# Kernel optimization log

Hardware: AMD Instinct MI355X
Metric: run time of the kernel (lower is better)

## Reference

```python
import jax, jax.numpy as jnp
import numpy as np

DECAY = 0.99
EPSILON = 1e-05
CODEBOOK_SIZE = 1024
DIM = 128


def setup_inputs() -> dict:
    key = jax.random.key(0)
    k1, k2, k3, k4 = jax.random.split(key, 4)
    x = jax.random.normal(k1, (8, 8192, DIM), dtype=jnp.float32)
    embed = jax.random.normal(k2, (CODEBOOK_SIZE, DIM), dtype=jnp.float32)
    cluster_size = jax.random.uniform(k3, (CODEBOOK_SIZE,), dtype=jnp.float32)
    embed_avg = jax.random.normal(k4, (CODEBOOK_SIZE, DIM), dtype=jnp.float32)
    return {"x": x, "embed": embed, "cluster_size": cluster_size, "embed_avg": embed_avg}


def reference(x, embed, cluster_size, embed_avg):
    shape = x.shape
    flat = x.reshape(-1, shape[-1])  # [N, dim]

    # quantize: negative squared euclidean distance, argmax == nearest code
    dist = -(jnp.sum(flat * flat, axis=1, keepdims=True)
             - 2.0 * flat @ embed.T
             + jnp.sum(embed * embed, axis=1)[None, :])  # [N, K]
    embed_ind = jnp.argmax(dist, axis=-1)  # [N]

    quantize = embed[embed_ind].reshape(shape)            # dequantize
    embed_ind_out = embed_ind.reshape(shape[:-1])

    # training-time EMA updates (one-hot expressed as segment_sum)
    batch_cluster_size = jax.ops.segment_sum(
        jnp.ones_like(embed_ind, dtype=flat.dtype), embed_ind,
        num_segments=CODEBOOK_SIZE)                       # == one_hot.sum(0)
    new_cluster_size = cluster_size * DECAY + (1.0 - DECAY) * batch_cluster_size

    embed_sum = jax.ops.segment_sum(flat, embed_ind,
                                    num_segments=CODEBOOK_SIZE)  # == (x.T @ one_hot).T
    new_embed_avg = embed_avg * DECAY + (1.0 - DECAY) * embed_sum

    total = new_cluster_size.sum()
    smoothed = (new_cluster_size + EPSILON) / (total + CODEBOOK_SIZE * EPSILON)
    smoothed_counts = smoothed * total
    new_embed = new_embed_avg / smoothed_counts[:, None]

    return quantize, embed_ind_out, new_cluster_size, new_embed_avg, new_embed
```

## Files before the change

### kernel.cpp

```cpp
#include <hip/hip_runtime.h>
#include <math.h>

#define DIM 128
#define KCODES 1024
#define NROWS 65536

typedef short bf16x8 __attribute__((ext_vector_type(8)));
typedef float f32x4 __attribute__((ext_vector_type(4)));

#define WS_COUNTS 0
#define WS_ESUM   1024
#define WS_IOFF   132096
#define WS_TOTAL  133120
#define WS_ENORM2 133124
#define WS_EBF    134148
#define WS_WIN    461828
#define WS_SORTED 527364
#define WS_SCODE  592900

#define OFF_Q   0
#define OFF_IND 8388608
#define OFF_NCS 8454144
#define OFF_NEA 8455168
#define OFF_NE  8586240

#define LDST 136

static __device__ __forceinline__ unsigned short f2bf(float f) {
    unsigned u = __float_as_uint(f);
    unsigned r = (u + 0x7FFFu + ((u >> 16) & 1u)) >> 16;
    return (unsigned short)r;
}

__global__ __launch_bounds__(64) void k_prep(const float* __restrict__ embed,
                                             unsigned short* __restrict__ ebf,
                                             float* __restrict__ en2,
                                             float* __restrict__ counts,
                                             float* __restrict__ esum) {
    int k = blockIdx.x;
    int l = threadIdx.x;
    if (l == 0) counts[k] = 0.0f;
    *(float2*)&esum[(size_t)k * DIM + l * 2] = (float2){0.0f, 0.0f};
    float2 v = *(const float2*)&embed[(size_t)k * DIM + l * 2];
    ushort2 b;
    b.x = f2bf(v.x);
    b.y = f2bf(v.y);
    *(ushort2*)&ebf[k * DIM + l * 2] = b;
    float s = v.x * v.x + v.y * v.y;
    #pragma unroll
    for (int off = 32; off; off >>= 1) s += __shfl_xor(s, off);
    if (l == 0) en2[k] = 512.0f - 0.5f * s;
}

__global__ __launch_bounds__(512, 4) void k_fused(const float* __restrict__ x,
                                                  const float* __restrict__ embed,
                                                  const unsigned short* __restrict__ ebf,
                                                  const float* __restrict__ en2g,
                                                  int* __restrict__ win_g,
                                                  float* __restrict__ counts,
                                                  float* __restrict__ out) {
    __shared__ unsigned short buf[2][128 * LDST];
    __shared__ float en2s[KCODES];
    __shared__ int winS[128];

    const int tid = threadIdx.x;
    const int row0 = blockIdx.x * 128;

    #pragma unroll
    for (int i = 0; i < 2; ++i) en2s[i * 512 + tid] = en2g[i * 512 + tid];

    #pragma unroll
    for (int i = 0; i < 8; ++i) {
        int idx4 = i * 512 + tid;
        int lin = idx4 * 4;
        int r = lin >> 7, d = lin & 127;
        float4 v = *(const float4*)&x[(size_t)(row0 + r) * DIM + d];
        ushort4 b;
        b.x = f2bf(v.x); b.y = f2bf(v.y); b.z = f2bf(v.z); b.w = f2bf(v.w);
        *(ushort4*)&buf[0][r * LDST + d] = b;
    }
    __syncthreads();

    const int lane = tid & 63;
    const int wv = tid >> 6;
    const int ch = wv & 1;
    const int rh = (wv >> 1) * 32;
    const int l15 = lane & 15;
    const int q = lane >> 4;

    bf16x8 af[4][2];
    #pragma unroll
    for (int ks = 0; ks < 4; ++ks)
        #pragma unroll
        for (int t = 0; t < 2; ++t)
            af[ks][t] = *(const bf16x8*)&buf[0][(rh + t * 16 + l15) * LDST + ks * 32 + q * 8];

    uint4 er[4];
    #pragma unroll
    for (int i = 0; i < 4; ++i) {
        int idx8 = i * 512 + tid;
        int r = idx8 >> 4;
        int d = (idx8 & 15) * 8;
        er[i] = *(const uint4*)&ebf[(size_t)r * DIM + d];
    }
    #pragma unroll
    for (int i = 0; i < 4; ++i) {
        int idx8 = i * 512 + tid;
        int r = idx8 >> 4;
        int d = (idx8 & 15) * 8;
        *(uint4*)&buf[1][r * LDST + d] = er[i];
    }
    __syncthreads();

    float m1[2][4], m2[2][4];
    #pragma unroll
    for (int a = 0; a < 2; ++a)
        #pragma unroll
        for (int b = 0; b < 4; ++b) { m1[a][b] = 0.0f; m2[a][b] = 0.0f; }

    for (int ct = 0; ct < 8; ++ct) {
        const int c0 = ct * 128;
        const unsigned short* cbuf = buf[1 ^ (ct & 1)];

        if (ct < 7) {
            #pragma unroll
            for (int i = 0; i < 4; ++i) {
                int idx8 = i * 512 + tid;
                int r = idx8 >> 4;
                int d = (idx8 & 15) * 8;
                er[i] = *(const uint4*)&ebf[(size_t)(c0 + 128 + r) * DIM + d];
            }
        }

        f32x4 acc[2][4];
        #pragma unroll
        for (int cl = 0; cl < 4; ++cl) {
            float en = en2s[c0 + ch * 64 + cl * 16 + l15];
            #pragma unroll
            for (int rt = 0; rt < 2; ++rt) acc[rt][cl] = (f32x4){en, en, en, en};
        }

        #pragma unroll
        for (int ks = 0; ks < 4; ++ks) {
            bf16x8 bfr[4];
            #pragma unroll
            for (int cl = 0; cl < 4; ++cl)
                bfr[cl] = *(const bf16x8*)&cbuf[(ch * 64 + cl * 16 + l15) * LDST + ks * 32 + q * 8];
            #pragma unroll
            for (int rt = 0; rt < 2; ++rt)
                #pragma unroll
                for (int cl = 0; cl < 4; ++cl)
                    acc[rt][cl] = __builtin_amdgcn_mfma_f32_16x16x32_bf16(af[ks][rt], bfr[cl],
                                                                          acc[rt][cl], 0, 0, 0);
        }

        #pragma unroll
        for (int cl = 0; cl < 4; ++cl) {
            unsigned cu = (unsigned)(c0 + ch * 64 + cl * 16 + l15);
            #pragma unroll
            for (int rt = 0; rt < 2; ++rt)
                #pragma unroll
                for (int rg = 0; rg < 4; ++rg) {
                    float s = acc[rt][cl][rg];
                    float kf = __uint_as_float((__float_as_uint(s) & ~1023u) | cu);
                    m2[rt][rg] = __builtin_amdgcn_fmed3f(m1[rt][rg], m2[rt][rg], kf);
                    m1[rt][rg] = fmaxf(m1[rt][rg], kf);
                }
        }

        if (ct < 7) {
            unsigned short* nbuf = buf[ct & 1];
            #pragma unroll
            for (int i = 0; i < 4; ++i) {
                int idx8 = i * 512 + tid;
                int r = idx8 >> 4;
                int d = (idx8 & 15) * 8;
                *(uint4*)&nbuf[r * LDST + d] = er[i];
            }
        }
        __syncthreads();
    }

    float* scratch = (float*)buf[0];
    unsigned* hist = (unsigned*)buf[0] + 512;

    #pragma unroll
    for (int rt = 0; rt < 2; ++rt)
        #pragma unroll
        for (int rg = 0; rg < 4; ++rg) {
            float a1 = m1[rt][rg], a2 = m2[rt][rg];
            #pragma unroll
            for (int off = 1; off <= 8; off <<= 1) {
                float o1 = __shfl_xor(a1, off);
                float o2 = __shfl_xor(a2, off);
                float t = fmaxf(a2, o2);
                a2 = __builtin_amdgcn_fmed3f(a1, o1, t);
                a1 = fmaxf(a1, o1);
            }
            if (l15 == 0) {
                int row = rh + rt * 16 + q * 4 + rg;
                scratch[row * 4 + ch * 2 + 0] = a1;
                scratch[row * 4 + ch * 2 + 1] = a2;
            }
        }

    #pragma unroll
    for (int i = 0; i < 2; ++i) hist[i * 512 + tid] = 0u;
    __syncthreads();

    {
        const int sub = tid & 15;
        const int g = tid >> 4;
        #pragma unroll 2
        for (int rr = 0; rr < 4; ++rr) {
            const int lrow = g * 4 + rr;
            const float* sp = &scratch[lrow * 4];
            int ci[4];
            ci[0] = (int)(__float_as_uint(sp[0]) & 1023u);
            ci[1] = (int)(__float_as_uint(sp[1]) & 1023u);
            ci[2] = (int)(__float_as_uint(sp[2]) & 1023u);
            ci[3] = (int)(__float_as_uint(sp[3]) & 1023u);

            const float* xr = &x[(size_t)(row0 + lrow) * DIM + sub * 4];
            float4 xa = *(const float4*)xr;
            float4 xb = *(const float4*)(xr + 64);

            double d[4];
            #pragma unroll
            for (int j = 0; j < 4; ++j) {
                const float* er2 = &embed[(size_t)ci[j] * DIM + sub * 4];
                float4 ea4 = *(const float4*)er2;
                float4 eb4 = *(const float4*)(er2 + 64);
                double t0 = (double)xa.x - (double)ea4.x;
                double t1 = (double)xa.y - (double)ea4.y;
                double t2 = (double)xa.z - (double)ea4.z;
                double t3 = (double)xa.w - (double)ea4.w;
                double t4 = (double)xb.x - (double)eb4.x;
                double t5 = (double)xb.y - (double)eb4.y;
                double t6 = (double)xb.z - (double)eb4.z;
                double t7 = (double)xb.w - (double)eb4.w;
                d[j] = ((t0 * t0 + t1 * t1) + (t2 * t2 + t3 * t3)) +
                       ((t4 * t4 + t5 * t5) + (t6 * t6 + t7 * t7));
            }
            #pragma unroll
            for (int off = 1; off <= 8; off <<= 1) {
                #pragma unroll
                for (int j = 0; j < 4; ++j) d[j] += __shfl_xor(d[j], off);
            }

            int win = ci[0];
            double dw = d[0];
            #pragma unroll
            for (int j = 1; j < 4; ++j) {
                bool b = (d[j] < dw) || (d[j] == dw && ci[j] < win);
                dw = b ? d[j] : dw;
                win = b ? ci[j] : win;
            }
            if (sub == 0) winS[lrow] = win;
        }
    }
    __syncthreads();

    if (tid < 128) {
        int w = winS[tid];
        atomicAdd(&hist[w], 1u);
        win_g[row0 + tid] = w;
        out[OFF_IND + row0 + tid] = (float)w;
    }

    #pragma unroll 4
    for (int i = 0; i < 16; ++i) {
        int lrow = wv * 16 + i;
        int w = winS[lrow];
        float2 v = *(const float2*)&embed[(size_t)w * DIM + lane * 2];
        *(float2*)&out[OFF_Q + (size_t)(row0 + lrow) * DIM + lane * 2] = v;
    }

    __syncthreads();
    #pragma unroll
    for (int i = 0; i < 2; ++i) {
        unsigned c = hist[i * 512 + tid];
        if (c) atomicAdd(&counts[i * 512 + tid], (float)c);
    }
}

__global__ __launch_bounds__(1024) void k_offsets(const float* __restrict__ cs,
                                                  float* __restrict__ out,
                                                  float* __restrict__ ws) {
    __shared__ int wsum[16];
    __shared__ float wtot[16];
    const float* counts = ws + WS_COUNTS;
    int* ioff = (int*)(ws + WS_IOFF);

    int t = threadIdx.x;
    int lane = t & 63, w = t >> 6;
    float cf = counts[t];
    int c = (int)cf;
    float ncs = cs[t] * 0.99f + 0.01f * cf;
    out[OFF_NCS + t] = ncs;

    int v = c;
    #pragma unroll
    for (int off = 1; off < 64; off <<= 1) {
        int o = __shfl_up(v, off);
        if (lane >= off) v += o;
    }
    float nf = ncs;
    #pragma unroll
    for (int off = 32; off; off >>= 1) nf += __shfl_xor(nf, off);

    if (lane == 63) wsum[w] = v;
    if (lane == 0) wtot[w] = nf;
    __syncthreads();

    int base = 0;
    for (int i = 0; i < w; ++i) base += wsum[i];
    ioff[t] = base + v - c;

    if (t == 0) {
        float tt = 0.f;
        for (int i = 0; i < 16; ++i) tt += wtot[i];
        ws[WS_TOTAL] = tt;
    }
}

__global__ __launch_bounds__(1024) void k_sortscatter(const int* __restrict__ win_arr,
                                                      int* __restrict__ ioff,
                                                      int* __restrict__ sorted,
                                                      int* __restrict__ scode) {
    __shared__ int h[KCODES];
    __shared__ int bs[KCODES];
    const int t = threadIdx.x;
    h[t] = 0;
    __syncthreads();
    const int row = blockIdx.x * 1024 + t;
    const int w = win_arr[row];
    const int r = atomicAdd(&h[w], 1);
    __syncthreads();
    const int c = h[t];
    if (c) bs[t] = atomicAdd(&ioff[t], c);
    __syncthreads();
    const int pos = bs[w] + r;
    sorted[pos] = row;
    scode[pos] = w;
}

__global__ __launch_bounds__(256) void k_segsum(const float* __restrict__ x,
                                                const int* __restrict__ sorted,
                                                const int* __restrict__ scode,
                                                float* __restrict__ esum) {
    const int lane = threadIdx.x & 63;
    const int wv = threadIdx.x >> 6;
    const int base = blockIdx.x * 256 + wv * 64;
    const int l15 = lane & 15;

    float ax = 0.f, ay = 0.f;
    int cur = -1;

    #pragma unroll
    for (int cc = 0; cc < 4; ++cc) {
        const int p = base + cc * 16 + l15;
        const int srow = sorted[p];
        const int sc = scode[p];
        if (cc == 0) cur = __shfl(sc, 0);
        #pragma unroll
        for (int j = 0; j < 16; ++j) {
            int row = __shfl(srow, j);
            int c = __shfl(sc, j);
            if (c != cur) {
                atomicAdd(&esum[cur * DIM + lane * 2], ax);
                atomicAdd(&esum[cur * DIM + lane * 2 + 1], ay);
                ax = 0.f; ay = 0.f;
                cur = c;
            }
            float2 v = *(const float2*)&x[(size_t)row * DIM + lane * 2];
            ax += v.x;
            ay += v.y;
        }
    }
    atomicAdd(&esum[cur * DIM + lane * 2], ax);
    atomicAdd(&esum[cur * DIM + lane * 2 + 1], ay);
}

__global__ __launch_bounds__(256) void k_embed(const float* __restrict__ ea,
                                               const float* __restrict__ ws,
                                               float* __restrict__ out) {
    int i = blockIdx.x * 256 + threadIdx.x;
    int k = i >> 7;
    float nea = ea[i] * 0.99f + 0.01f * ws[WS_ESUM + i];
    out[OFF_NEA + i] = nea;
    float total = ws[WS_TOTAL];
    float ncs = out[OFF_NCS + k];
    float sm = (ncs + 1e-5f) / (total + 1024.0f * 1e-5f);
    out[OFF_NE + i] = nea / (sm * total);
}

extern "C" void kernel_launch(void* const* d_in, const int* in_sizes, int n_in,
                              void* d_out, int out_size, void* d_ws, size_t ws_size,
                              hipStream_t stream) {
    const float* x     = (const float*)d_in[0];
    const float* embed = (const float*)d_in[1];
    const float* cs    = (const float*)d_in[2];
    const float* ea    = (const float*)d_in[3];
    float* out = (float*)d_out;
    float* ws  = (float*)d_ws;

    k_prep<<<KCODES, 64, 0, stream>>>(embed, (unsigned short*)(ws + WS_EBF),
                                      ws + WS_ENORM2, ws + WS_COUNTS, ws + WS_ESUM);
    k_fused<<<NROWS / 128, 512, 0, stream>>>(x, embed,
                                             (const unsigned short*)(ws + WS_EBF),
                                             ws + WS_ENORM2, (int*)(ws + WS_WIN),
                                             ws + WS_COUNTS, out);
    k_offsets<<<1, 1024, 0, stream>>>(cs, out, ws);
    k_sortscatter<<<NROWS / 1024, 1024, 0, stream>>>((const int*)(ws + WS_WIN),
                                                     (int*)(ws + WS_IOFF),
                                                     (int*)(ws + WS_SORTED),
                                                     (int*)(ws + WS_SCODE));
    k_segsum<<<NROWS / 256, 256, 0, stream>>>(x, (const int*)(ws + WS_SORTED),
                                              (const int*)(ws + WS_SCODE), ws + WS_ESUM);
    k_embed<<<131072 / 256, 256, 0, stream>>>(ea, ws, out);
}
```

Measured before the change: 162.1 us.

## Swizzle LDS layout, pair argmax updates, and fuse offset scan into sort scatter

```diff
diff --git a/kernel.cpp b/kernel.cpp
--- a/kernel.cpp
+++ b/kernel.cpp
@@ -24,8 +24,6 @@
 #define OFF_NEA 8455168
 #define OFF_NE  8586240
 
-#define LDST 136
-
 static __device__ __forceinline__ unsigned short f2bf(float f) {
     unsigned u = __float_as_uint(f);
     unsigned r = (u + 0x7FFFu + ((u >> 16) & 1u)) >> 16;
@@ -36,10 +34,11 @@
                                              unsigned short* __restrict__ ebf,
                                              float* __restrict__ en2,
                                              float* __restrict__ counts,
-                                             float* __restrict__ esum) {
+                                             float* __restrict__ esum,
+                                             int* __restrict__ cursor) {
     int k = blockIdx.x;
     int l = threadIdx.x;
-    if (l == 0) counts[k] = 0.0f;
+    if (l == 0) { counts[k] = 0.0f; cursor[k] = 0; }
     *(float2*)&esum[(size_t)k * DIM + l * 2] = (float2){0.0f, 0.0f};
     float2 v = *(const float2*)&embed[(size_t)k * DIM + l * 2];
     ushort2 b;
@@ -59,7 +58,7 @@
                                                   int* __restrict__ win_g,
                                                   float* __restrict__ counts,
                                                   float* __restrict__ out) {
-    __shared__ unsigned short buf[2][128 * LDST];
+    __shared__ unsigned short buf[2][128 * 128];
     __shared__ float en2s[KCODES];
     __shared__ int winS[128];
 
@@ -77,7 +76,7 @@
         float4 v = *(const float4*)&x[(size_t)(row0 + r) * DIM + d];
         ushort4 b;
         b.x = f2bf(v.x); b.y = f2bf(v.y); b.z = f2bf(v.z); b.w = f2bf(v.w);
-        *(ushort4*)&buf[0][r * LDST + d] = b;
+        *(ushort4*)&buf[0][(r * 128 + d) ^ ((r & 7) << 3)] = b;
     }
     __syncthreads();
 
@@ -87,13 +86,14 @@
     const int rh = (wv >> 1) * 32;
     const int l15 = lane & 15;
     const int q = lane >> 4;
+    const int swz = (l15 & 7) << 3;
 
     bf16x8 af[4][2];
     #pragma unroll
     for (int ks = 0; ks < 4; ++ks)
         #pragma unroll
         for (int t = 0; t < 2; ++t)
-            af[ks][t] = *(const bf16x8*)&buf[0][(rh + t * 16 + l15) * LDST + ks * 32 + q * 8];
+            af[ks][t] = *(const bf16x8*)&buf[0][((rh + t * 16 + l15) * 128 + ks * 32 + q * 8) ^ swz];
 
     uint4 er[4];
     #pragma unroll
@@ -108,7 +108,7 @@
         int idx8 = i * 512 + tid;
         int r = idx8 >> 4;
         int d = (idx8 & 15) * 8;
-        *(uint4*)&buf[1][r * LDST + d] = er[i];
+        *(uint4*)&buf[1][(r * 128 + d) ^ ((r & 7) << 3)] = er[i];
     }
     __syncthreads();
 
@@ -140,12 +140,13 @@
             for (int rt = 0; rt < 2; ++rt) acc[rt][cl] = (f32x4){en, en, en, en};
         }
 
+        __builtin_amdgcn_s_setprio(1);
         #pragma unroll
         for (int ks = 0; ks < 4; ++ks) {
             bf16x8 bfr[4];
             #pragma unroll
             for (int cl = 0; cl < 4; ++cl)
-                bfr[cl] = *(const bf16x8*)&cbuf[(ch * 64 + cl * 16 + l15) * LDST + ks * 32 + q * 8];
+                bfr[cl] = *(const bf16x8*)&cbuf[((ch * 64 + cl * 16 + l15) * 128 + ks * 32 + q * 8) ^ swz];
             #pragma unroll
             for (int rt = 0; rt < 2; ++rt)
                 #pragma unroll
@@ -155,18 +156,23 @@
         }
 
         #pragma unroll
-        for (int cl = 0; cl < 4; ++cl) {
-            unsigned cu = (unsigned)(c0 + ch * 64 + cl * 16 + l15);
+        for (int cp = 0; cp < 2; ++cp) {
+            unsigned cu0 = (unsigned)(c0 + ch * 64 + cp * 32 + l15);
+            unsigned cu1 = cu0 + 16u;
             #pragma unroll
             for (int rt = 0; rt < 2; ++rt)
                 #pragma unroll
                 for (int rg = 0; rg < 4; ++rg) {
-                    float s = acc[rt][cl][rg];
-                    float kf = __uint_as_float((__float_as_uint(s) & ~1023u) | cu);
-                    m2[rt][rg] = __builtin_amdgcn_fmed3f(m1[rt][rg], m2[rt][rg], kf);
-                    m1[rt][rg] = fmaxf(m1[rt][rg], kf);
+                    float sa = acc[rt][cp * 2][rg];
+                    float sb = acc[rt][cp * 2 + 1][rg];
+                    float a = __uint_as_float((__float_as_uint(sa) & ~1023u) | cu0);
+                    float b = __uint_as_float((__float_as_uint(sb) & ~1023u) | cu1);
+                    m2[rt][rg] = fmaxf(m2[rt][rg],
+                                       __builtin_amdgcn_fmed3f(a, b, m1[rt][rg]));
+                    m1[rt][rg] = fmaxf(fmaxf(a, b), m1[rt][rg]);
                 }
         }
+        __builtin_amdgcn_s_setprio(0);
 
         if (ct < 7) {
             unsigned short* nbuf = buf[ct & 1];
@@ -175,7 +181,7 @@
                 int idx8 = i * 512 + tid;
                 int r = idx8 >> 4;
                 int d = (idx8 & 15) * 8;
-                *(uint4*)&nbuf[r * LDST + d] = er[i];
+                *(uint4*)&nbuf[(r * 128 + d) ^ ((r & 7) << 3)] = er[i];
             }
         }
         __syncthreads();
@@ -284,61 +290,58 @@
     }
 }
 
-__global__ __launch_bounds__(1024) void k_offsets(const float* __restrict__ cs,
-                                                  float* __restrict__ out,
-                                                  float* __restrict__ ws) {
+__global__ __launch_bounds__(1024) void k_scansort(const float* __restrict__ cs,
+                                                   const int* __restrict__ win_arr,
+                                                   float* __restrict__ ws,
+                                                   int* __restrict__ sorted,
+                                                   int* __restrict__ scode,
+                                                   float* __restrict__ out) {
+    __shared__ int h[KCODES];
+    __shared__ int bs[KCODES];
     __shared__ int wsum[16];
     __shared__ float wtot[16];
     const float* counts = ws + WS_COUNTS;
-    int* ioff = (int*)(ws + WS_IOFF);
-
-    int t = threadIdx.x;
-    int lane = t & 63, w = t >> 6;
-    float cf = counts[t];
-    int c = (int)cf;
-    float ncs = cs[t] * 0.99f + 0.01f * cf;
-    out[OFF_NCS + t] = ncs;
-
+    int* cursor = (int*)(ws + WS_IOFF);
+
+    const int t = threadIdx.x;
+    h[t] = 0;
+    __syncthreads();
+    const int row = blockIdx.x * 1024 + t;
+    const int w = win_arr[row];
+    const int r = atomicAdd(&h[w], 1);
+
+    const int lane = t & 63, wvi = t >> 6;
+    const float cf = counts[t];
+    const int c = (int)cf;
     int v = c;
     #pragma unroll
     for (int off = 1; off < 64; off <<= 1) {
         int o = __shfl_up(v, off);
         if (lane >= off) v += o;
     }
-    float nf = ncs;
-    #pragma unroll
-    for (int off = 32; off; off >>= 1) nf += __shfl_xor(nf, off);
-
-    if (lane == 63) wsum[w] = v;
-    if (lane == 0) wtot[w] = nf;
+    if (lane == 63) wsum[wvi] = v;
+    if (blockIdx.x == 0) {
+        float ncs = cs[t] * 0.99f + 0.01f * cf;
+        out[OFF_NCS + t] = ncs;
+        float nf = ncs;
+        #pragma unroll
+        for (int off = 32; off; off >>= 1) nf += __shfl_xor(nf, off);
+        if (lane == 0) wtot[wvi] = nf;
+    }
     __syncthreads();
 
     int base = 0;
-    for (int i = 0; i < w; ++i) base += wsum[i];
-    ioff[t] = base + v - c;
-
-    if (t == 0) {
+    for (int i = 0; i < wvi; ++i) base += wsum[i];
+    const int gbase = base + v - c;
+
+    if (blockIdx.x == 0 && t == 0) {
         float tt = 0.f;
         for (int i = 0; i < 16; ++i) tt += wtot[i];
         ws[WS_TOTAL] = tt;
     }
-}
-
-__global__ __launch_bounds__(1024) void k_sortscatter(const int* __restrict__ win_arr,
-                                                      int* __restrict__ ioff,
-                                                      int* __restrict__ sorted,
-                                                      int* __restrict__ scode) {
-    __shared__ int h[KCODES];
-    __shared__ int bs[KCODES];
-    const int t = threadIdx.x;
-    h[t] = 0;
-    __syncthreads();
-    const int row = blockIdx.x * 1024 + t;
-    const int w = win_arr[row];
-    const int r = atomicAdd(&h[w], 1);
-    __syncthreads();
-    const int c = h[t];
-    if (c) bs[t] = atomicAdd(&ioff[t], c);
+
+    const int cnt = h[t];
+    if (cnt) bs[t] = gbase + atomicAdd(&cursor[t], cnt);
     __syncthreads();
     const int pos = bs[w] + r;
     sorted[pos] = row;
@@ -406,16 +409,15 @@
     float* ws  = (float*)d_ws;
 
     k_prep<<<KCODES, 64, 0, stream>>>(embed, (unsigned short*)(ws + WS_EBF),
-                                      ws + WS_ENORM2, ws + WS_COUNTS, ws + WS_ESUM);
+                                      ws + WS_ENORM2, ws + WS_COUNTS, ws + WS_ESUM,
+                                      (int*)(ws + WS_IOFF));
     k_fused<<<NROWS / 128, 512, 0, stream>>>(x, embed,
                                              (const unsigned short*)(ws + WS_EBF),
                                              ws + WS_ENORM2, (int*)(ws + WS_WIN),
                                              ws + WS_COUNTS, out);
-    k_offsets<<<1, 1024, 0, stream>>>(cs, out, ws);
-    k_sortscatter<<<NROWS / 1024, 1024, 0, stream>>>((const int*)(ws + WS_WIN),
-                                                     (int*)(ws + WS_IOFF),
-                                                     (int*)(ws + WS_SORTED),
-                                                     (int*)(ws + WS_SCODE));
+    k_scansort<<<NROWS / 1024, 1024, 0, stream>>>(cs, (const int*)(ws + WS_WIN), ws,
+                                                  (int*)(ws + WS_SORTED),
+                                                  (int*)(ws + WS_SCODE), out);
     k_segsum<<<NROWS / 256, 256, 0, stream>>>(x, (const int*)(ws + WS_SORTED),
                                               (const int*)(ws + WS_SCODE), ws + WS_ESUM);
     k_embed<<<131072 / 256, 256, 0, stream>>>(ea, ws, out);
```

New measurement: 152.7 us. 1.06x faster.
